# Kernel optimization log

Hardware: AMD Instinct MI355X
Metric: run time of the kernel (lower is better)

Reference implementation:

```python
import jax, jax.numpy as jnp
import numpy as np

B, N, D = 8, 1024, 1024
H, DH = 16, 64
INNER = H * DH  # == D by construction
MLP = 4096
EPS = 1e-5


def layernorm(x, g, b):
    mu = jnp.mean(x, axis=-1, keepdims=True)
    var = jnp.mean(jnp.square(x - mu), axis=-1, keepdims=True)
    return (x - mu) * jax.lax.rsqrt(var + EPS) * g + b


def setup_inputs() -> dict:
    key = jax.random.key(0)
    ks = jax.random.split(key, 10)
    s = lambda fan_in: 1.0 / np.sqrt(fan_in)
    return {
        "x": jax.random.normal(ks[0], (B, N, D), jnp.float32),
        "ln1_g": jnp.ones((D,), jnp.float32),
        "ln1_b": jnp.zeros((D,), jnp.float32),
        "w_qkv": jax.random.uniform(ks[1], (D, 3 * INNER), jnp.float32, -s(D), s(D)),
        "w_out": jax.random.uniform(ks[2], (INNER, D), jnp.float32, -s(INNER), s(INNER)),
        "b_out": jnp.zeros((D,), jnp.float32),
        "ln2_g": jnp.ones((D,), jnp.float32),
        "ln2_b": jnp.zeros((D,), jnp.float32),
        "w1": jax.random.uniform(ks[3], (D, MLP), jnp.float32, -s(D), s(D)),
        "b1": jnp.zeros((MLP,), jnp.float32),
        "w2": jax.random.uniform(ks[4], (MLP, D), jnp.float32, -s(MLP), s(MLP)),
        "b2": jnp.zeros((D,), jnp.float32),
    }


def reference(x, ln1_g, ln1_b, w_qkv, w_out, b_out, ln2_g, ln2_b, w1, b1, w2, b2):
    scale = DH ** -0.5
    xn = layernorm(x, ln1_g, ln1_b)
    qkv = xn @ w_qkv  # [B, N, 3*INNER]
    embed_dim = xn.shape[-1]
    # faithful to source: slice by embed_dim (== INNER here)
    q, k, v = (qkv[:, :, embed_dim * i: embed_dim * (i + 1)] for i in range(3))
    reshape_heads = lambda t: t.reshape(B, N, H, DH).transpose(0, 2, 1, 3)  # b h n d
    q, k, v = reshape_heads(q), reshape_heads(k), reshape_heads(v)
    scores = jnp.einsum("bhnd,bhmd->bhnm", q, k) * scale
    attn = jax.nn.softmax(scores, axis=-1)
    attn_out = jnp.einsum("bhnm,bhmd->bhnd", attn, v)
    attn_out = attn_out.transpose(0, 2, 1, 3).reshape(B, N, INNER)
    x2 = attn_out @ w_out + b_out  # to_ff projection (project_out=True)
    # feed_forward: LayerNorm -> Linear -> GELU(exact) -> Linear (dropout=0)
    h = layernorm(x2, ln2_g, ln2_b) @ w1 + b1
    h = jax.nn.gelu(h, approximate=False)
    out = h @ w2 + b2
    return out
```

## Files before the change

kernel.cpp:

```cpp
#include <hip/hip_runtime.h>
#include <hip/hip_bf16.h>
#include <math.h>

typedef __bf16 bf16;
typedef __bf16 bf16x8 __attribute__((ext_vector_type(8)));
typedef float f32x4 __attribute__((ext_vector_type(4)));

#define SEQ 1024
#define DMODEL 1024

__device__ __forceinline__ void gld_lds16(const bf16* g, bf16* l) {
    __builtin_amdgcn_global_load_lds(
        (const __attribute__((address_space(1))) unsigned int*)g,
        (__attribute__((address_space(3))) unsigned int*)l, 16, 0, 0);
}

__global__ void transpose_f2b(const float* __restrict__ in, bf16* __restrict__ out,
                              int K, int N) {
    __shared__ float tile[32][33];
    int n0 = blockIdx.x * 32, k0 = blockIdx.y * 32;
    int tx = threadIdx.x, ty = threadIdx.y;
#pragma unroll
    for (int i = 0; i < 4; ++i) {
        int kk = ty + i * 8;
        tile[kk][tx] = in[(size_t)(k0 + kk) * N + n0 + tx];
    }
    __syncthreads();
#pragma unroll
    for (int i = 0; i < 4; ++i) {
        int nn = ty + i * 8;
        out[(size_t)(n0 + nn) * K + k0 + tx] = (bf16)tile[tx][nn];
    }
}

__global__ void ln_f2b(const float* __restrict__ x, const float* __restrict__ g,
                       const float* __restrict__ bta, bf16* __restrict__ y) {
    int row = blockIdx.x, t = threadIdx.x;
    const float* xr = x + (size_t)row * DMODEL;
    float v[4];
#pragma unroll
    for (int i = 0; i < 4; ++i) v[i] = xr[t * 4 + i];
    float s = v[0] + v[1] + v[2] + v[3];
    float s2 = v[0] * v[0] + v[1] * v[1] + v[2] * v[2] + v[3] * v[3];
#pragma unroll
    for (int off = 32; off > 0; off >>= 1) {
        s += __shfl_down(s, off, 64);
        s2 += __shfl_down(s2, off, 64);
    }
    __shared__ float ws1[4], ws2[4];
    __shared__ float mu_s, rstd_s;
    int lane = t & 63, wv = t >> 6;
    if (lane == 0) { ws1[wv] = s; ws2[wv] = s2; }
    __syncthreads();
    if (t == 0) {
        float S1 = ws1[0] + ws1[1] + ws1[2] + ws1[3];
        float S2 = ws2[0] + ws2[1] + ws2[2] + ws2[3];
        float mu = S1 * (1.0f / DMODEL);
        float var = S2 * (1.0f / DMODEL) - mu * mu;
        mu_s = mu;
        rstd_s = rsqrtf(var + 1e-5f);
    }
    __syncthreads();
    float mu = mu_s, rstd = rstd_s;
    bf16* yr = y + (size_t)row * DMODEL;
#pragma unroll
    for (int i = 0; i < 4; ++i) {
        int d = t * 4 + i;
        float o = (v[i] - mu) * rstd * g[d] + bta[d];
        yr[d] = (bf16)o;
    }
}

#define BM 128
#define BN 128
#define BK 32

__global__ __launch_bounds__(256, 2) void gemm_bt(
    const bf16* __restrict__ A, const bf16* __restrict__ Bt,
    const float* __restrict__ bias, void* __restrict__ Cv,
    int M, int N, int K, int mode) {
    __shared__ bf16 sA[BM * BK];
    __shared__ bf16 sB[BN * BK];
    int t = threadIdx.x;
    int lane = t & 63, wave = t >> 6;
    int wr = wave >> 1, wc = wave & 1;
    int m0 = blockIdx.y * BM, n0 = blockIdx.x * BN;
    const bf16* Ap = A + (size_t)m0 * K;
    const bf16* Bp = Bt + (size_t)n0 * K;

    int srow = wave * 16 + (lane >> 2);
    int schunk = lane & 3;
    int gcoff = (schunk ^ (srow & 3)) * 8;
    const bf16* gA0 = Ap + (size_t)srow * K + gcoff;
    const bf16* gA1 = Ap + (size_t)(srow + 64) * K + gcoff;
    const bf16* gB0 = Bp + (size_t)srow * K + gcoff;
    const bf16* gB1 = Bp + (size_t)(srow + 64) * K + gcoff;
    bf16* lA0 = sA + wave * 512;
    bf16* lA1 = sA + 2048 + wave * 512;
    bf16* lB0 = sB + wave * 512;
    bf16* lB1 = sB + 2048 + wave * 512;

    f32x4 acc[4][4];
#pragma unroll
    for (int i = 0; i < 4; ++i)
#pragma unroll
        for (int j = 0; j < 4; ++j) acc[i][j] = (f32x4){0.f, 0.f, 0.f, 0.f};

    int mq = lane & 15, quad = lane >> 4;
    int csw = (quad ^ (mq & 3)) * 8;

    for (int k0 = 0; k0 < K; k0 += BK) {
        __syncthreads();
        gld_lds16(gA0 + k0, lA0);
        gld_lds16(gA1 + k0, lA1);
        gld_lds16(gB0 + k0, lB0);
        gld_lds16(gB1 + k0, lB1);
        __syncthreads();
        bf16x8 af[4], bfr[4];
#pragma unroll
        for (int i = 0; i < 4; ++i)
            af[i] = *(const bf16x8*)&sA[(wr * 64 + i * 16 + mq) * BK + csw];
#pragma unroll
        for (int j = 0; j < 4; ++j)
            bfr[j] = *(const bf16x8*)&sB[(wc * 64 + j * 16 + mq) * BK + csw];
#pragma unroll
        for (int i = 0; i < 4; ++i)
#pragma unroll
            for (int j = 0; j < 4; ++j)
                acc[i][j] = __builtin_amdgcn_mfma_f32_16x16x32_bf16(af[i], bfr[j], acc[i][j], 0, 0, 0);
    }

    int cq = lane & 15, rq = (lane >> 4) * 4;
#pragma unroll
    for (int i = 0; i < 4; ++i) {
        int row = m0 + wr * 64 + i * 16 + rq;
#pragma unroll
        for (int j = 0; j < 4; ++j) {
            int col = n0 + wc * 64 + j * 16 + cq;
            float bv = bias ? bias[col] : 0.0f;
#pragma unroll
            for (int r = 0; r < 4; ++r) {
                float v = acc[i][j][r] + bv;
                if (mode == 1) v = 0.5f * v * (1.0f + erff(v * 0.70710678118654752f));
                size_t idx = (size_t)(row + r) * N + col;
                if (mode == 2) ((float*)Cv)[idx] = v;
                else           ((bf16*)Cv)[idx] = (bf16)v;
            }
        }
    }
}

#define GBAR() do { asm volatile("" ::: "memory"); __builtin_amdgcn_sched_barrier(0); \
    __builtin_amdgcn_s_barrier(); __builtin_amdgcn_sched_barrier(0); asm volatile("" ::: "memory"); } while (0)
#define GWAITV2() do { asm volatile("s_waitcnt vmcnt(2)" ::: "memory"); __builtin_amdgcn_sched_barrier(0); } while (0)
#define GWAITV0() do { asm volatile("s_waitcnt vmcnt(0)" ::: "memory"); __builtin_amdgcn_sched_barrier(0); } while (0)

__global__ __launch_bounds__(512, 2) void gemm256_bt(
    const bf16* __restrict__ A, const bf16* __restrict__ Bt,
    const float* __restrict__ bias, void* __restrict__ Cv,
    int M, int N, int K, int mode) {
    extern __shared__ bf16 smem[];
    int t = threadIdx.x;
    int lane = t & 63, wave = t >> 6;
    int wr = wave >> 2, wc = wave & 3;

    int nbx = gridDim.x;
    int nwg = nbx * (int)gridDim.y;
    int bid = (int)blockIdx.y * nbx + (int)blockIdx.x;
    int qd = nwg >> 3, rm = nwg & 7;
    int xcd = bid & 7, loc = bid >> 3;
    int wg = (xcd < rm ? xcd * (qd + 1) : rm * (qd + 1) + (xcd - rm) * qd) + loc;
    int m0 = (wg / nbx) * 256, n0 = (wg % nbx) * 256;

    const bf16* Ap = A + (size_t)m0 * K;
    const bf16* Bp = Bt + (size_t)n0 * K;

    int sr = lane >> 3;
    int g8 = lane & 7;
    int soff = (g8 ^ (sr & 7)) * 8;
    const bf16* gA = Ap + (size_t)(wave * 8 + sr) * K + soff;
    const bf16* gB = Bp + (size_t)(wave * 8 + sr) * K + soff;

    int mq = lane & 15, quad = lane >> 4;
    int fro = (quad ^ (mq & 7)) * 8;

    f32x4 acc[8][4];
#pragma unroll
    for (int i = 0; i < 8; ++i)
#pragma unroll
        for (int j = 0; j < 4; ++j) acc[i][j] = (f32x4){0.f, 0.f, 0.f, 0.f};

    bf16x8 af[4][2], bq[2][2];
    const bf16 *sA, *sB;
    int nt = K >> 6;

#define SMP(b, ab) (smem + ((size_t)((b) * 2 + (ab))) * 16384)
#define STG(b, cl, tt) do { \
    gld_lds16(gA + (size_t)(cl) * 64 * K + (size_t)(tt) * 64, SMP(b, 0) + ((cl) * 64 + wave * 8) * 64); \
    gld_lds16(gB + (size_t)(cl) * 64 * K + (size_t)(tt) * 64, SMP(b, 1) + ((cl) * 64 + wave * 8) * 64); \
} while (0)
#define LDA(ih) do { _Pragma("unroll") for (int i = 0; i < 4; ++i) { \
    int rw = wr * 128 + (ih) * 64 + i * 16 + mq; \
    af[i][0] = *(const bf16x8*)&sA[rw * 64 + fro]; \
    af[i][1] = *(const bf16x8*)&sA[rw * 64 + (fro ^ 32)]; } } while (0)
#define LDB(jh) do { _Pragma("unroll") for (int j = 0; j < 2; ++j) { \
    int rw = wc * 64 + (jh) * 32 + j * 16 + mq; \
    bq[j][0] = *(const bf16x8*)&sB[rw * 64 + fro]; \
    bq[j][1] = *(const bf16x8*)&sB[rw * 64 + (fro ^ 32)]; } } while (0)
#define MM(ih, jh) do { __builtin_amdgcn_s_setprio(1); \
    _Pragma("unroll") for (int j = 0; j < 2; ++j) \
    _Pragma("unroll") for (int i = 0; i < 4; ++i) { \
        acc[(ih) * 4 + i][(jh) * 2 + j] = __builtin_amdgcn_mfma_f32_16x16x32_bf16( \
            af[i][0], bq[j][0], acc[(ih) * 4 + i][(jh) * 2 + j], 0, 0, 0); \
        acc[(ih) * 4 + i][(jh) * 2 + j] = __builtin_amdgcn_mfma_f32_16x16x32_bf16( \
            af[i][1], bq[j][1], acc[(ih) * 4 + i][(jh) * 2 + j], 0, 0, 0); } \
    __builtin_amdgcn_s_setprio(0); } while (0)

#pragma unroll
    for (int cl = 0; cl < 4; ++cl) STG(0, cl, 0);
    if (nt > 1) { STG(1, 0, 1); GWAITV2(); } else { GWAITV0(); }
    GBAR();

    for (int tt = 0; tt < nt; ++tt) {
        int b = tt & 1;
        sA = SMP(b, 0);
        sB = SMP(b, 1);
        int pf = (tt + 1 < nt);
        LDA(0); LDB(0);
        if (pf) STG(b ^ 1, 1, tt + 1);
        GBAR();
        MM(0, 0);
        GBAR();
        LDB(1);
        if (pf) STG(b ^ 1, 2, tt + 1);
        GBAR();
        MM(0, 1);
        GBAR();
        LDA(1);
        if (pf) STG(b ^ 1, 3, tt + 1);
        GBAR();
        MM(1, 1);
        GBAR();
        LDB(0);
        GBAR();
        MM(1, 0);
        GBAR();
        if (pf) {
            if (tt + 2 < nt) { STG(b, 0, tt + 2); GWAITV2(); }
            else             { GWAITV0(); }
            GBAR();
        }
    }

#undef SMP
#undef STG
#undef LDA
#undef LDB
#undef MM

    int cq = lane & 15, rq = (lane >> 4) * 4;
#pragma unroll
    for (int i = 0; i < 8; ++i) {
        int row = m0 + wr * 128 + i * 16 + rq;
#pragma unroll
        for (int j = 0; j < 4; ++j) {
            int col = n0 + wc * 64 + j * 16 + cq;
            float bv = bias ? bias[col] : 0.0f;
#pragma unroll
            for (int r = 0; r < 4; ++r) {
                float v = acc[i][j][r] + bv;
                if (mode == 1) v = 0.5f * v * (1.0f + erff(v * 0.70710678118654752f));
                size_t idx = (size_t)(row + r) * N + col;
                if (mode == 2) ((float*)Cv)[idx] = v;
                else           ((bf16*)Cv)[idx] = (bf16)v;
            }
        }
    }
}

#define LDK 72

__global__ __launch_bounds__(256, 2) void attn_mfma(const bf16* __restrict__ qkv,
                                                    bf16* __restrict__ ao) {
    __shared__ bf16 Klds[64][LDK];
    __shared__ bf16 Vtlds[64][LDK];
    __shared__ bf16 Plds[4][16][LDK];
    int t = threadIdx.x, lane = t & 63, wave = t >> 6;
    int bh = blockIdx.y, bb = bh >> 4, h = bh & 15;
    int q0 = blockIdx.x * 64;
    const bf16* base = qkv + (size_t)bb * SEQ * 3072;
    int m = lane & 15, quad = lane >> 4;
    int kq = quad * 8;

    bf16x8 qf[2];
    {
        int qrow = q0 + wave * 16 + m;
        const bf16* p = base + (size_t)qrow * 3072 + h * 64;
#pragma unroll
        for (int c = 0; c < 2; ++c) {
            bf16x8 tmp = *(const bf16x8*)(p + c * 32 + kq);
#pragma unroll
            for (int j = 0; j < 8; ++j) qf[c][j] = (bf16)((float)tmp[j] * 0.125f);
        }
    }

    float m_run[4], l_run[4];
    f32x4 o_acc[4];
#pragma unroll
    for (int r = 0; r < 4; ++r) { m_run[r] = -3e38f; l_run[r] = 0.f; }
#pragma unroll
    for (int g = 0; g < 4; ++g) o_acc[g] = (f32x4){0.f, 0.f, 0.f, 0.f};

    int skey = t >> 3, sd0 = (t & 7) * 8;
    int rot = t & 7;

    for (int kt = 0; kt < 16; ++kt) {
        __syncthreads();
        {
            const bf16* pk = base + (size_t)(kt * 64 + skey) * 3072 + 1024 + h * 64 + sd0;
            *(bf16x8*)&Klds[skey][sd0]      = *(const bf16x8*)pk;
            *(bf16x8*)&Klds[skey + 32][sd0] = *(const bf16x8*)(pk + 32 * 3072);
            const bf16* pv = base + (size_t)(kt * 64 + skey) * 3072 + 2048 + h * 64 + sd0;
            bf16x8 v0 = *(const bf16x8*)pv;
            bf16x8 v1 = *(const bf16x8*)(pv + 32 * 3072);
#pragma unroll
            for (int ii = 0; ii < 8; ++ii) {
                int j = (ii + rot) & 7;
                Vtlds[sd0 + j][skey]      = v0[j];
                Vtlds[sd0 + j][skey + 32] = v1[j];
            }
        }
        __syncthreads();

        f32x4 s[4];
#pragma unroll
        for (int g = 0; g < 4; ++g) {
            bf16x8 b0 = *(const bf16x8*)&Klds[g * 16 + m][kq];
            bf16x8 b1 = *(const bf16x8*)&Klds[g * 16 + m][32 + kq];
            s[g] = (f32x4){0.f, 0.f, 0.f, 0.f};
            s[g] = __builtin_amdgcn_mfma_f32_16x16x32_bf16(qf[0], b0, s[g], 0, 0, 0);
            s[g] = __builtin_amdgcn_mfma_f32_16x16x32_bf16(qf[1], b1, s[g], 0, 0, 0);
        }

#pragma unroll
        for (int r = 0; r < 4; ++r) {
            float mx = fmaxf(fmaxf(s[0][r], s[1][r]), fmaxf(s[2][r], s[3][r]));
#pragma unroll
            for (int msk = 1; msk < 16; msk <<= 1) mx = fmaxf(mx, __shfl_xor(mx, msk, 64));
            float m_new = fmaxf(m_run[r], mx);
            float alpha = __expf(m_run[r] - m_new);
            m_run[r] = m_new;
            float rowsum = 0.f;
#pragma unroll
            for (int g = 0; g < 4; ++g) {
                float p = __expf(s[g][r] - m_new);
                s[g][r] = p;
                rowsum += p;
            }
#pragma unroll
            for (int msk = 1; msk < 16; msk <<= 1) rowsum += __shfl_xor(rowsum, msk, 64);
            l_run[r] = l_run[r] * alpha + rowsum;
#pragma unroll
            for (int g = 0; g < 4; ++g) o_acc[g][r] *= alpha;
        }

#pragma unroll
        for (int g = 0; g < 4; ++g)
#pragma unroll
            for (int r = 0; r < 4; ++r)
                Plds[wave][quad * 4 + r][g * 16 + m] = (bf16)s[g][r];

#pragma unroll
        for (int kc = 0; kc < 2; ++kc) {
            bf16x8 pf = *(const bf16x8*)&Plds[wave][m][kc * 32 + kq];
#pragma unroll
            for (int dg = 0; dg < 4; ++dg) {
                bf16x8 vf = *(const bf16x8*)&Vtlds[dg * 16 + m][kc * 32 + kq];
                o_acc[dg] = __builtin_amdgcn_mfma_f32_16x16x32_bf16(pf, vf, o_acc[dg], 0, 0, 0);
            }
        }
    }

#pragma unroll
    for (int r = 0; r < 4; ++r) {
        int row = q0 + wave * 16 + quad * 4 + r;
        float rl = 1.0f / l_run[r];
        bf16* op = ao + ((size_t)bb * SEQ + row) * DMODEL + h * 64;
#pragma unroll
        for (int g = 0; g < 4; ++g) op[g * 16 + m] = (bf16)(o_acc[g][r] * rl);
    }
}

extern "C" void kernel_launch(void* const* d_in, const int* in_sizes, int n_in,
                              void* d_out, int out_size, void* d_ws, size_t ws_size,
                              hipStream_t stream) {
    const float* x     = (const float*)d_in[0];
    const float* ln1_g = (const float*)d_in[1];
    const float* ln1_b = (const float*)d_in[2];
    const float* w_qkv = (const float*)d_in[3];
    const float* w_out = (const float*)d_in[4];
    const float* b_out = (const float*)d_in[5];
    const float* ln2_g = (const float*)d_in[6];
    const float* ln2_b = (const float*)d_in[7];
    const float* w1    = (const float*)d_in[8];
    const float* b1    = (const float*)d_in[9];
    const float* w2    = (const float*)d_in[10];
    const float* b2    = (const float*)d_in[11];
    float* out = (float*)d_out;
    char* ws = (char*)d_ws;
    char* outc = (char*)d_out;

    static bool lds_init = false;
    if (!lds_init) {
        hipFuncSetAttribute((const void*)gemm256_bt,
                            hipFuncAttributeMaxDynamicSharedMemorySize, 131072);
        lds_init = true;
    }

    bf16* wqkvT = (bf16*)(ws + (0ull << 20));
    bf16* woutT = (bf16*)(ws + (6ull << 20));
    bf16* qkv   = (bf16*)(ws + (8ull << 20));
    bf16* w1T   = (bf16*)(ws + (8ull << 20));
    bf16* w2T   = (bf16*)(ws + (16ull << 20));
    float* x2   = (float*)(ws + (24ull << 20));
    bf16* hbuf  = (bf16*)(ws + (24ull << 20));
    bf16* xn    = (bf16*)(outc + 0);
    bf16* ao    = (bf16*)(outc + 0);
    bf16* x2n   = (bf16*)(outc + (16ull << 20));

    dim3 tb(32, 8);
    transpose_f2b<<<dim3(3072 / 32, 1024 / 32), tb, 0, stream>>>(w_qkv, wqkvT, 1024, 3072);
    transpose_f2b<<<dim3(1024 / 32, 1024 / 32), tb, 0, stream>>>(w_out, woutT, 1024, 1024);

    ln_f2b<<<8192, 256, 0, stream>>>(x, ln1_g, ln1_b, xn);
    gemm256_bt<<<dim3(3072 / 256, 8192 / 256), 512, 131072, stream>>>(xn, wqkvT, nullptr, qkv,
                                                                      8192, 3072, 1024, 0);
    attn_mfma<<<dim3(SEQ / 64, 128), 256, 0, stream>>>(qkv, ao);

    transpose_f2b<<<dim3(4096 / 32, 1024 / 32), tb, 0, stream>>>(w1, w1T, 1024, 4096);
    transpose_f2b<<<dim3(1024 / 32, 4096 / 32), tb, 0, stream>>>(w2, w2T, 4096, 1024);

    gemm_bt<<<dim3(1024 / 128, 8192 / 128), 256, 0, stream>>>(ao, woutT, b_out, x2,
                                                              8192, 1024, 1024, 2);
    ln_f2b<<<8192, 256, 0, stream>>>(x2, ln2_g, ln2_b, x2n);

    for (int c = 0; c < 2; ++c) {
        const bf16* a1 = x2n + (size_t)c * 4096 * 1024;
        float* oc = out + (size_t)c * 4096 * 1024;
        gemm256_bt<<<dim3(4096 / 256, 4096 / 256), 512, 131072, stream>>>(a1, w1T, b1, hbuf,
                                                                          4096, 4096, 1024, 1);
        gemm_bt<<<dim3(1024 / 128, 4096 / 128), 256, 0, stream>>>(hbuf, w2T, b2, oc,
                                                                  4096, 1024, 4096, 2);
    }
}
```

Baseline: 698.4 us.

## Enlarge attention KV tile to 128, prefetch next tile into registers, remap blocks

The attention kernel now processes 128 keys per iteration instead of 64, halving the number of loop iterations and barriers. The next K/V tile is loaded into registers while the current tile's MFMAs run, then written to LDS after a barrier, overlapping global latency with compute. Block indices are also remapped so that consecutive workgroups are spread across (batch, head, query) in a strided order, presumably to improve L2/XCD locality. The cost is more registers (kreg/vreg, 8 score fragments) and more LDS, which could reduce occupancy at the 2-blocks-per-CU bound.

```diff
diff --git a/kernel.cpp b/kernel.cpp
--- a/kernel.cpp
+++ b/kernel.cpp
@@ -278,16 +278,22 @@
     }
 }
 
-#define LDK 72
+#define KVB 128
+#define LDK2 72
+#define LDP 136
 
 __global__ __launch_bounds__(256, 2) void attn_mfma(const bf16* __restrict__ qkv,
                                                     bf16* __restrict__ ao) {
-    __shared__ bf16 Klds[64][LDK];
-    __shared__ bf16 Vtlds[64][LDK];
-    __shared__ bf16 Plds[4][16][LDK];
+    __shared__ bf16 Klds[KVB][LDK2];
+    __shared__ bf16 Vtlds[64][LDP];
+    __shared__ bf16 Plds[4][16][LDP];
     int t = threadIdx.x, lane = t & 63, wave = t >> 6;
-    int bh = blockIdx.y, bb = bh >> 4, h = bh & 15;
-    int q0 = blockIdx.x * 64;
+
+    int f = (int)blockIdx.y * (int)gridDim.x + (int)blockIdx.x;
+    int wg = (f & 7) * 256 + (f >> 3);
+    int bh = wg >> 4, bb = bh >> 4, h = bh & 15;
+    int q0 = (wg & 15) * 64;
+
     const bf16* base = qkv + (size_t)bb * SEQ * 3072;
     int m = lane & 15, quad = lane >> 4;
     int kq = quad * 8;
@@ -313,28 +319,36 @@
 
     int skey = t >> 3, sd0 = (t & 7) * 8;
     int rot = t & 7;
-
-    for (int kt = 0; kt < 16; ++kt) {
-        __syncthreads();
-        {
-            const bf16* pk = base + (size_t)(kt * 64 + skey) * 3072 + 1024 + h * 64 + sd0;
-            *(bf16x8*)&Klds[skey][sd0]      = *(const bf16x8*)pk;
-            *(bf16x8*)&Klds[skey + 32][sd0] = *(const bf16x8*)(pk + 32 * 3072);
-            const bf16* pv = base + (size_t)(kt * 64 + skey) * 3072 + 2048 + h * 64 + sd0;
-            bf16x8 v0 = *(const bf16x8*)pv;
-            bf16x8 v1 = *(const bf16x8*)(pv + 32 * 3072);
-#pragma unroll
-            for (int ii = 0; ii < 8; ++ii) {
-                int j = (ii + rot) & 7;
-                Vtlds[sd0 + j][skey]      = v0[j];
-                Vtlds[sd0 + j][skey + 32] = v1[j];
-            }
-        }
-        __syncthreads();
-
-        f32x4 s[4];
-#pragma unroll
-        for (int g = 0; g < 4; ++g) {
+    const bf16* pk0 = base + (size_t)skey * 3072 + 1024 + h * 64 + sd0;
+    const bf16* pv0 = base + (size_t)skey * 3072 + 2048 + h * 64 + sd0;
+
+    bf16x8 kreg[4], vreg[4];
+
+#define LOADKV(kt2) do { \
+    const bf16* pk = pk0 + (size_t)(kt2) * KVB * 3072; \
+    const bf16* pv = pv0 + (size_t)(kt2) * KVB * 3072; \
+    _Pragma("unroll") for (int c = 0; c < 4; ++c) { \
+        kreg[c] = *(const bf16x8*)(pk + (size_t)c * 32 * 3072); \
+        vreg[c] = *(const bf16x8*)(pv + (size_t)c * 32 * 3072); } \
+} while (0)
+#define WRITEKV() do { \
+    _Pragma("unroll") for (int c = 0; c < 4; ++c) { \
+        *(bf16x8*)&Klds[skey + c * 32][sd0] = kreg[c]; \
+        _Pragma("unroll") for (int ii = 0; ii < 8; ++ii) { \
+            int j = (ii + rot) & 7; \
+            Vtlds[sd0 + j][skey + c * 32] = vreg[c][j]; } } \
+} while (0)
+
+    LOADKV(0);
+    WRITEKV();
+    __syncthreads();
+
+    for (int kt = 0; kt < SEQ / KVB; ++kt) {
+        if (kt + 1 < SEQ / KVB) LOADKV(kt + 1);
+
+        f32x4 s[8];
+#pragma unroll
+        for (int g = 0; g < 8; ++g) {
             bf16x8 b0 = *(const bf16x8*)&Klds[g * 16 + m][kq];
             bf16x8 b1 = *(const bf16x8*)&Klds[g * 16 + m][32 + kq];
             s[g] = (f32x4){0.f, 0.f, 0.f, 0.f};
@@ -344,7 +358,9 @@
 
 #pragma unroll
         for (int r = 0; r < 4; ++r) {
-            float mx = fmaxf(fmaxf(s[0][r], s[1][r]), fmaxf(s[2][r], s[3][r]));
+            float mx = s[0][r];
+#pragma unroll
+            for (int g = 1; g < 8; ++g) mx = fmaxf(mx, s[g][r]);
 #pragma unroll
             for (int msk = 1; msk < 16; msk <<= 1) mx = fmaxf(mx, __shfl_xor(mx, msk, 64));
             float m_new = fmaxf(m_run[r], mx);
@@ -352,7 +368,7 @@
             m_run[r] = m_new;
             float rowsum = 0.f;
 #pragma unroll
-            for (int g = 0; g < 4; ++g) {
+            for (int g = 0; g < 8; ++g) {
                 float p = __expf(s[g][r] - m_new);
                 s[g][r] = p;
                 rowsum += p;
@@ -365,13 +381,13 @@
         }
 
 #pragma unroll
-        for (int g = 0; g < 4; ++g)
+        for (int g = 0; g < 8; ++g)
 #pragma unroll
             for (int r = 0; r < 4; ++r)
                 Plds[wave][quad * 4 + r][g * 16 + m] = (bf16)s[g][r];
 
 #pragma unroll
-        for (int kc = 0; kc < 2; ++kc) {
+        for (int kc = 0; kc < 4; ++kc) {
             bf16x8 pf = *(const bf16x8*)&Plds[wave][m][kc * 32 + kq];
 #pragma unroll
             for (int dg = 0; dg < 4; ++dg) {
@@ -379,7 +395,16 @@
                 o_acc[dg] = __builtin_amdgcn_mfma_f32_16x16x32_bf16(pf, vf, o_acc[dg], 0, 0, 0);
             }
         }
-    }
+
+        __syncthreads();
+        if (kt + 1 < SEQ / KVB) {
+            WRITEKV();
+        }
+        __syncthreads();
+    }
+
+#undef LOADKV
+#undef WRITEKV
 
 #pragma unroll
     for (int r = 0; r < 4; ++r) {
```

Measured after the change: 697.6 us. Within noise of the previous version (-0.1%).
